# Kernel tuning notes

Measured on AMD Instinct MI355X. Metric: run time of the kernel, lower is better.

## Reference

```python
import jax, jax.numpy as jnp
import numpy as np

B, S, DIN, DOUT = 4, 2048, 4096, 4096

def setup_inputs() -> dict:
    key = jax.random.key(0)
    k1, k2, k3 = jax.random.split(key, 3)
    x = jax.random.normal(k1, (B, S, DIN), dtype=jnp.float32)
    # kaiming-uniform-like scale for weight, uniform bias in [-1/sqrt(fan_in), 1/sqrt(fan_in)]
    bound_w = 1.0 / np.sqrt(DIN)
    weight = jax.random.uniform(k2, (DOUT, DIN), minval=-bound_w, maxval=bound_w, dtype=jnp.float32)
    bias = jax.random.uniform(k3, (DOUT,), minval=-bound_w, maxval=bound_w, dtype=jnp.float32)
    kk = jnp.asarray(1.0, dtype=jnp.float32)
    aa = jnp.asarray(1.0, dtype=jnp.float32)
    return {"x": x, "weight": weight, "bias": bias, "kk": kk, "aa": aa}

def reference(x, weight, bias, kk, aa):
    # Adiabatic binarization: soft-binarize weight with w_b = aa * tanh(kk * w),
    # then standard linear y = x @ w_b.T + bias. As kk -> inf, w_b -> aa*sign(w).
    w_b = aa * jnp.tanh(kk * weight)          # [DOUT, DIN]
    y = jnp.einsum('bsi,oi->bso', x, w_b)     # [B, S, DOUT]
    return y + bias
```

## Files before the change

kernel.cpp:

```cpp
#include <hip/hip_runtime.h>
#include <stdint.h>

#define B_DIM 4
#define S_DIM 2048
#define DIN   4096
#define DOUT  4096
#define M_TOT (B_DIM * S_DIM)

typedef __attribute__((ext_vector_type(8))) short  bf16x8;
typedef __attribute__((ext_vector_type(4))) float  f32x4;
typedef __attribute__((ext_vector_type(4))) unsigned short u16x4;
typedef __attribute__((ext_vector_type(4))) float  float4v;

__device__ __forceinline__ unsigned short f2b(float f) {
  union { float f; unsigned int i; } v; v.f = f;
  unsigned int r = v.i + 0x7FFFu + ((v.i >> 16) & 1u);
  return (unsigned short)(r >> 16);
}

__global__ void cvt_fused_kernel(const float4v* __restrict__ w, u16x4* __restrict__ wbo,
                                 const float4v* __restrict__ x, u16x4* __restrict__ xbo,
                                 const float* __restrict__ kk,
                                 const float* __restrict__ aa) {
  const int bid = blockIdx.x;
  if (bid < 2048) {
    const float k = kk[0];
    const float a = aa[0];
    const int n4 = DOUT * DIN / 4;
    for (int i = bid * 256 + threadIdx.x; i < n4; i += 2048 * 256) {
      float4v v = w[i];
      u16x4 o;
#pragma unroll
      for (int j = 0; j < 4; ++j) o[j] = f2b(a * tanhf(k * v[j]));
      wbo[i] = o;
    }
  } else {
    const int n4 = M_TOT * DIN / 4;
    for (int i = (bid - 2048) * 256 + threadIdx.x; i < n4; i += 4096 * 256) {
      float4v v = x[i];
      u16x4 o;
#pragma unroll
      for (int j = 0; j < 4; ++j) o[j] = f2b(v[j]);
      xbo[i] = o;
    }
  }
}

#define BM 256
#define BN 256
#define BK 64
#define NT (DIN / BK)

__device__ __forceinline__ void glds16(const unsigned short* g, unsigned short* l) {
  __builtin_amdgcn_global_load_lds(
      (const __attribute__((address_space(1))) void*)g,
      (__attribute__((address_space(3))) void*)l,
      16, 0, 0);
}

#define BARX()    __builtin_amdgcn_s_barrier()
#define LGKM0()   asm volatile("s_waitcnt lgkmcnt(0)" ::: "memory")
#define WAITVM4() asm volatile("s_waitcnt vmcnt(4)" ::: "memory")
#define WAITVM0() asm volatile("s_waitcnt vmcnt(0)" ::: "memory")

#define RDB(dst, BLK, BUFB)                                                   \
  dst[0] = *(const bf16x8*)(bRd + (BUFB) + 0 * 2048 + (BLK));                 \
  dst[1] = *(const bf16x8*)(bRd + (BUFB) + 1 * 2048 + (BLK));                 \
  dst[2] = *(const bf16x8*)(bRd + (BUFB) + 2 * 2048 + (BLK));                 \
  dst[3] = *(const bf16x8*)(bRd + (BUFB) + 3 * 2048 + (BLK));

#define RDA4(dst, MB, BLK, BUFB)                                              \
  dst[0] = *(const bf16x8*)(aRd + (BUFB) + ((MB) + 0) * 2048 + (BLK));        \
  dst[1] = *(const bf16x8*)(aRd + (BUFB) + ((MB) + 1) * 2048 + (BLK));        \
  dst[2] = *(const bf16x8*)(aRd + (BUFB) + ((MB) + 2) * 2048 + (BLK));        \
  dst[3] = *(const bf16x8*)(aRd + (BUFB) + ((MB) + 3) * 2048 + (BLK));

#define MFMA_PH(AF, BF, MB)                                                   \
  __builtin_amdgcn_s_setprio(1);                                              \
  {                                                                           \
    _Pragma("unroll")                                                         \
    for (int i = 0; i < 4; ++i)                                               \
      _Pragma("unroll")                                                       \
      for (int ni = 0; ni < 4; ++ni)                                          \
        acc[(MB) + i][ni] = __builtin_amdgcn_mfma_f32_16x16x32_bf16(          \
            AF[i], BF[ni], acc[(MB) + i][ni], 0, 0, 0);                       \
  }                                                                           \
  __builtin_amdgcn_s_setprio(0);

#define KTILE(t, BUFB)                                                        \
  {                                                                           \
                         \
    RDB(bfr0, blk0, BUFB);                                                    \
    RDA4(afA, 0, blk0, BUFB);                                                 \
    stageAh((t) + 1, 0);                                                      \
    BARX(); LGKM0();                                                          \
    MFMA_PH(afA, bfr0, 0);                                                    \
    BARX();                                                                   \
           \
    RDA4(afB, 4, blk0, BUFB);                                                 \
    RDB(bfr1, blk1, BUFB);                                                    \
    stageAh((t) + 1, 1);                                                      \
    BARX(); LGKM0();                                                          \
    MFMA_PH(afB, bfr0, 4);                                                    \
    BARX();                                                                   \
                       \
    RDA4(afA, 0, blk1, BUFB);                                                 \
    RDA4(afB, 4, blk1, BUFB);                                                 \
    stageBh((t) + 2, 0);                                                      \
    BARX(); LGKM0();                                                          \
    MFMA_PH(afA, bfr1, 0);                                                    \
    BARX();                                                                   \
                   \
    stageBh((t) + 2, 1);                                                      \
    MFMA_PH(afB, bfr1, 4);                                                    \
    if ((t) + 2 < NT) { WAITVM4(); } else { WAITVM0(); }                      \
    BARX();                                                                   \
  }

__global__ __launch_bounds__(512, 2)
void gemm256_kernel(const unsigned short* __restrict__ A,
                    const unsigned short* __restrict__ Bw,
                    const float* __restrict__ bias,
                    float* __restrict__ C) {
  __shared__ unsigned short lds[2][2][BM * BK];

  const int tid  = threadIdx.x;
  const int wv   = tid >> 6;
  const int lane = tid & 63;
  const int l15  = lane & 15;
  const int quad = lane >> 4;
  const int l7   = lane & 7;
  const int rlan = lane >> 3;

  const int xcd = blockIdx.x & 7;
  const int idx = blockIdx.x >> 3;
  const int bm  = ((((xcd & 3) << 3) | (idx & 7)) << 8);
  const int bn  = ((((xcd >> 2) << 3) | (idx >> 3)) << 8);

  const unsigned short* aLane = A  + (size_t)(bm + wv * 16 + rlan) * DIN + ((l7 ^ rlan) << 3);
  const unsigned short* bLane = Bw + (size_t)(bn + wv * 16 + rlan) * DIN + ((l7 ^ rlan) << 3);

  auto stageAh = [&](int kt, int hr) {
    if (kt >= NT) return;
    const unsigned short* ga = aLane + (size_t)hr * (128 * DIN) + (size_t)kt * BK;
    unsigned short* la = &lds[kt & 1][0][hr * (128 * BK) + wv * (16 * BK)];
    glds16(ga, la);
    glds16(ga + 8 * DIN, la + 8 * BK);
  };
  auto stageBh = [&](int kt, int hr) {
    if (kt >= NT) return;
    const unsigned short* gb = bLane + (size_t)hr * (128 * DIN) + (size_t)kt * BK;
    unsigned short* lb = &lds[kt & 1][1][hr * (128 * BK) + wv * (16 * BK)];
    glds16(gb, lb);
    glds16(gb + 8 * DIN, lb + 8 * BK);
  };

  stageBh(0, 0); stageBh(0, 1); stageAh(0, 0); stageAh(0, 1);
  stageBh(1, 0); stageBh(1, 1);

  const int hA   = wv >> 2;
  const int hB   = (wv & 3) >> 1;
  const int wloc = wv & 1;
  const char* aRd = (const char*)&lds[0][0][0] + hA * 16384 + l15 * 128;
  const char* bRd = (const char*)&lds[0][1][0] + hB * 16384 + wloc * 8192 + l15 * 128;
  const int blk0 = ((0 + quad) ^ l7) * 16;
  const int blk1 = ((4 + quad) ^ l7) * 16;

  f32x4  acc[8][4] = {};
  bf16x8 bfr0[4], bfr1[4], afA[4], afB[4];

  WAITVM4();
  BARX();

#pragma unroll 1
  for (int t = 0; t < NT; t += 2) {
    KTILE(t, 0);
    KTILE(t + 1, 65536);
  }

  const int wm = (wv >> 2) * 128;
  const int wn = (wv & 3) * 64;
#pragma unroll
  for (int ni = 0; ni < 4; ++ni) {
    const int col = bn + wn + ni * 16 + l15;
    const float bv = bias[col];
#pragma unroll
    for (int mi = 0; mi < 8; ++mi) {
      const int row0 = bm + wm + mi * 16 + quad * 4;
#pragma unroll
      for (int e = 0; e < 4; ++e)
        C[(size_t)(row0 + e) * DOUT + col] = acc[mi][ni][e] + bv;
    }
  }
}

extern "C" void kernel_launch(void* const* d_in, const int* in_sizes, int n_in,
                              void* d_out, int out_size, void* d_ws, size_t ws_size,
                              hipStream_t stream) {
  const float* x    = (const float*)d_in[0];
  const float* w    = (const float*)d_in[1];
  const float* bias = (const float*)d_in[2];
  const float* kk   = (const float*)d_in[3];
  const float* aa   = (const float*)d_in[4];
  float* out = (float*)d_out;

  unsigned short* wb = (unsigned short*)d_ws;
  unsigned short* xb = wb + (size_t)DOUT * DIN;

  cvt_fused_kernel<<<6144, 256, 0, stream>>>(
      (const float4v*)w, (u16x4*)wb, (const float4v*)x, (u16x4*)xb, kk, aa);

  gemm256_kernel<<<dim3(512), dim3(512), 0, stream>>>(xb, wb, bias, out);
}
```

Measured before the change: 493.9 us.

## Software-pipeline LDS fragment reads across MFMA phases and drop per-phase barriers

Restructures the K-tile loop so the LDS fragment reads for the next MFMA phase are issued before the current phase, waiting on partial lgkmcnt counts instead of draining to zero. It also prefetches the first fragments of the next K-tile before the final phase. Most of the per-phase block barriers are removed, keeping two per tile, and sched_barrier stops the compiler from reordering the code. This aims to hide LDS latency behind MFMA work and cut synchronization stalls. The cost is more live registers and a tighter ordering between global staging and LDS reads across waves, which could race or spill.

```diff
diff --git a/kernel.cpp b/kernel.cpp
--- a/kernel.cpp
+++ b/kernel.cpp
@@ -59,7 +59,8 @@
 }
 
 #define BARX()    __builtin_amdgcn_s_barrier()
-#define LGKM0()   asm volatile("s_waitcnt lgkmcnt(0)" ::: "memory")
+#define SB0()     __builtin_amdgcn_sched_barrier(0)
+#define LGKMW(n)  asm volatile("s_waitcnt lgkmcnt(" #n ")" ::: "memory")
 #define WAITVM4() asm volatile("s_waitcnt vmcnt(4)" ::: "memory")
 #define WAITVM0() asm volatile("s_waitcnt vmcnt(0)" ::: "memory")
 
@@ -87,34 +88,34 @@
   }                                                                           \
   __builtin_amdgcn_s_setprio(0);
 
-#define KTILE(t, BUFB)                                                        \
+#define KTILE(t, BUFB, NBUFB)                                                 \
   {                                                                           \
-                         \
-    RDB(bfr0, blk0, BUFB);                                                    \
-    RDA4(afA, 0, blk0, BUFB);                                                 \
-    stageAh((t) + 1, 0);                                                      \
-    BARX(); LGKM0();                                                          \
+        \
+    stageAh((t) + 1, 0); stageAh((t) + 1, 1);                                 \
+    RDA4(afB, 4, blk0, BUFB);                                                 \
+    LGKMW(4); SB0();                                                          \
     MFMA_PH(afA, bfr0, 0);                                                    \
-    BARX();                                                                   \
-           \
-    RDA4(afB, 4, blk0, BUFB);                                                 \
+                                        \
+    RDA4(afA, 0, blk1, BUFB);                                                 \
     RDB(bfr1, blk1, BUFB);                                                    \
-    stageAh((t) + 1, 1);                                                      \
-    BARX(); LGKM0();                                                          \
+    LGKMW(8); SB0();                                                          \
     MFMA_PH(afB, bfr0, 4);                                                    \
-    BARX();                                                                   \
-                       \
-    RDA4(afA, 0, blk1, BUFB);                                                 \
+                                        \
     RDA4(afB, 4, blk1, BUFB);                                                 \
-    stageBh((t) + 2, 0);                                                      \
-    BARX(); LGKM0();                                                          \
+    LGKMW(4); SB0();                                                          \
     MFMA_PH(afA, bfr1, 0);                                                    \
-    BARX();                                                                   \
-                   \
-    stageBh((t) + 2, 1);                                                      \
+    BARX();             \
+       \
+    stageBh((t) + 2, 0); stageBh((t) + 2, 1);                                 \
+    if ((t) + 2 < NT) { WAITVM4(); } else { WAITVM0(); }                      \
+    BARX();                       \
+    if ((t) + 1 < NT) {                                                       \
+      RDA4(afA, 0, blk0, NBUFB);                                              \
+      RDB(bfr0, blk0, NBUFB);                                                 \
+    }                                                                         \
+    LGKMW(8); SB0();                                                          \
     MFMA_PH(afB, bfr1, 4);                                                    \
-    if ((t) + 2 < NT) { WAITVM4(); } else { WAITVM0(); }                      \
-    BARX();                                                                   \
+    BARX();          \
   }
 
 __global__ __launch_bounds__(512, 2)
@@ -155,9 +156,6 @@
     glds16(gb + 8 * DIN, lb + 8 * BK);
   };
 
-  stageBh(0, 0); stageBh(0, 1); stageAh(0, 0); stageAh(0, 1);
-  stageBh(1, 0); stageBh(1, 1);
-
   const int hA   = wv >> 2;
   const int hB   = (wv & 3) >> 1;
   const int wloc = wv & 1;
@@ -169,13 +167,17 @@
   f32x4  acc[8][4] = {};
   bf16x8 bfr0[4], bfr1[4], afA[4], afB[4];
 
+  stageBh(0, 0); stageBh(0, 1); stageAh(0, 0); stageAh(0, 1);
+  stageBh(1, 0); stageBh(1, 1);
   WAITVM4();
   BARX();
+  RDA4(afA, 0, blk0, 0);
+  RDB(bfr0, blk0, 0);
 
 #pragma unroll 1
   for (int t = 0; t < NT; t += 2) {
-    KTILE(t, 0);
-    KTILE(t + 1, 65536);
+    KTILE(t, 0, 65536);
+    KTILE(t + 1, 65536, 0);
   }
 
   const int wm = (wv >> 2) * 128;
```

Result: slower. 744.9 us (+50.8%).
